# Optimization experiments

Hardware: AMD Instinct MI355X
Metric: run time of the kernel (lower is better)

The kernel has to match this reference:

```python
import jax, jax.numpy as jnp
import numpy as np

B, C, CO = 8, 32, 32            # batch, in_channels, out_channels
NIN, NOUT, D1, D2 = 16, 10, 512, 512  # MLP dims: 16 -> 512 -> 512 -> 10 (L=3)
NRC = (NIN + 2 * NOUT + 6) * C  # rc_inp feature dim = 42*C = 1344


def _conv1(x, W, b):
    # 1x1 Conv1d: x (b, Cin, N) -> (b, Cout, N)
    return jnp.einsum('oi,bin->bon', W, x) + b[None, :, None]


def _lin(x, W, b):
    return x @ W.T + b


def setup_inputs() -> dict:
    key = jax.random.key(0)
    ks = iter(jax.random.split(key, 64))
    def rn(shape, s=1.0):
        return jax.random.normal(next(ks), shape, dtype=jnp.float32) * s
    return {
        'w0': rn((B, C, D1, NIN)), 'w1': rn((B, C, D2, D1)), 'w2': rn((B, C, NOUT, D2)),
        'b0': rn((B, C, D1)), 'b1': rn((B, C, D2)), 'b2': rn((B, C, NOUT)),
        'W_w0_rpt': rn((NIN * CO, (NIN + 2) * C), 0.02), 'B_w0_rpt': rn((NIN * CO,), 0.02),
        'W_w0_rc': rn((NIN * CO, NRC), 0.02), 'B_w0_rc': rn((NIN * CO,), 0.02),
        'W_b0': rn((CO, (NIN + 2) * C), 0.02), 'B_b0': rn((CO,), 0.02),
        'W_b0_rc': rn((CO, NRC), 0.02), 'B_b0_rc': rn((CO,), 0.02),
        'W_l1': rn((CO, C), 0.02), 'B_l1': rn((CO,), 0.02),
        'W_l1_rc': rn((CO, NRC), 0.02), 'B_l1_rc': rn((CO,), 0.02),
        'W_l1_r': rn((CO, (3 + NIN) * C), 0.02), 'B_l1_r': rn((CO,), 0.02),
        'W_l1_c': rn((CO, (3 + NOUT) * C), 0.02), 'B_l1_c': rn((CO,), 0.02),
        'W_bias1': rn((CO, (3 + NOUT) * C), 0.02), 'B_bias1': rn((CO,), 0.02),
        'W_bias1_rc': rn((CO, NRC), 0.02), 'B_bias1_rc': rn((CO,), 0.02),
        'W_fin_cpt': rn((NOUT * CO, (NOUT + 1) * C), 0.02), 'B_fin_cpt': rn((NOUT * CO,), 0.02),
        'W_fin_rc': rn((NOUT * CO, NRC), 0.02), 'B_fin_rc': rn((NOUT * CO,), 0.02),
        'W_bfin_rc': rn((NOUT * CO, NRC), 0.02), 'B_bfin_rc': rn((NOUT * CO,), 0.02),
    }


def reference(w0, w1, w2, b0, b1, b2,
              W_w0_rpt, B_w0_rpt, W_w0_rc, B_w0_rc, W_b0, B_b0, W_b0_rc, B_b0_rc,
              W_l1, B_l1, W_l1_rc, B_l1_rc, W_l1_r, B_l1_r, W_l1_c, B_l1_c,
              W_bias1, B_bias1, W_bias1_rc, B_bias1_rc,
              W_fin_cpt, B_fin_cpt, W_fin_rc, B_fin_rc, W_bfin_rc, B_bfin_rc):
    b = w0.shape[0]
    cm0, cm1, cm2 = w0.mean(-1), w1.mean(-1), w2.mean(-1)  # col means (b,c,n_row)
    rm0, rm1, rm2 = w0.mean(-2), w1.mean(-2), w2.mean(-2)  # row means (b,c,n_col)
    rc = jnp.concatenate([
        w0.mean((-1, -2)), w1.mean((-1, -2)), w2.mean((-1, -2)),
        b0.mean(-1), b1.mean(-1), b2.mean(-1),
        rm0.reshape(b, -1), cm2.reshape(b, -1), b2.reshape(b, -1)], axis=-1)  # (b, NRC)
    # ---- layer 0 (row-pointwise + rc broadcast) ----
    rpt = jnp.concatenate([jnp.swapaxes(w0, -1, -2).reshape(b, C * NIN, D1), rm1, b0], axis=1)
    z0 = _conv1(rpt, W_w0_rpt, B_w0_rpt) + _lin(rc, W_w0_rc, B_w0_rc)[..., None]
    zw0 = jnp.swapaxes(z0.reshape(b, CO, NIN, D1), -1, -2)  # (b, co, D1, NIN)
    u0 = _conv1(rpt, W_b0, B_b0) + _lin(rc, W_b0_rc, B_b0_rc)[..., None]  # (b, co, D1)
    # ---- middle layer (pointwise + rc + row + col broadcasts) ----
    row_b = jnp.concatenate([rm1, cm0, b0, jnp.swapaxes(w0, -1, -2).reshape(b, C * NIN, D1)], axis=1)
    col_b = jnp.concatenate([cm1, b1, rm2, w2.reshape(b, C * NOUT, D2)], axis=1)
    zw1 = (jnp.einsum('oi,bihw->bohw', W_l1, w1) + B_l1[None, :, None, None]
           + _lin(rc, W_l1_rc, B_l1_rc)[..., None, None]
           + _conv1(row_b, W_l1_r, B_l1_r)[:, :, None, :]
           + _conv1(col_b, W_l1_c, B_l1_c)[:, :, :, None])  # (b, co, D2, D1)
    u1 = _conv1(col_b, W_bias1, B_bias1) + _lin(rc, W_bias1_rc, B_bias1_rc)[..., None]  # (b, co, D2)
    # ---- final layer (col-pointwise + rc broadcast) ----
    cpt = jnp.concatenate([w2.reshape(b, C * NOUT, D2), cm1], axis=1)
    zf = _conv1(cpt, W_fin_cpt, B_fin_cpt) + _lin(rc, W_fin_rc, B_fin_rc)[..., None]
    zw2 = zf.reshape(b, CO, NOUT, D2)
    u2 = _lin(rc, W_bfin_rc, B_bfin_rc).reshape(b, CO, NOUT)
    return (zw0, zw1, zw2, u0, u1, u2)
```

## Files before the change

kernel.cpp:

```cpp
#include <hip/hip_runtime.h>

#define OUT_ZW1 2097152u
#define OUT_ZW2 69206016u
#define OUT_U0  70516736u
#define OUT_U1  70647808u
#define OUT_U2  70778880u

#define WS_RM1P   0u
#define WS_CM1    524288u
#define WS_CM0    655360u
#define WS_RM2    786432u
#define WS_RCW1   917504u
#define WS_RC     918528u
#define WS_RTERM  929280u
#define WS_CTERM  1060352u
#define WS_W0T    1191424u
#define WS_TW0    3288576u
#define WS_TB0    3292672u
#define WS_TL1    3292928u
#define WS_TBIAS1 3293184u
#define WS_TFIN   3293440u

static __device__ __forceinline__ float wave_reduce(float v) {
#pragma unroll
  for (int off = 32; off > 0; off >>= 1) v += __shfl_down(v, off);
  return v;
}

__global__ __launch_bounds__(256) void ksetup(
    const float* __restrict__ w0, const float* __restrict__ w2,
    const float* __restrict__ b0, const float* __restrict__ b1,
    const float* __restrict__ b2, const float* __restrict__ w1,
    float* __restrict__ ws) {
  __shared__ float sred[16];
  __shared__ float stot;
  __shared__ float rpart[512];
  __shared__ float swsum[4];
  int tid = threadIdx.x, lane = tid & 63;
  int bx = blockIdx.x;

  if (bx < 256) {
    int bc = bx;
    int b = bc >> 5, c = bc & 31;
    float* rcb = ws + WS_RC + b * 1344;
    float* cm0 = ws + WS_CM0;
    float* rm2 = ws + WS_RM2;

    if (tid < 16) sred[tid] = 0.f;
    if (tid == 0) stot = 0.f;
    __syncthreads();
    {
      float rm0p[16];
#pragma unroll
      for (int k = 0; k < 16; ++k) rm0p[k] = 0.f;
      float tot = 0.f;
      for (int d = tid; d < 512; d += 256) {
        const float4* p = (const float4*)(w0 + ((size_t)bc * 512 + d) * 16);
        float s = 0.f;
#pragma unroll
        for (int q = 0; q < 4; ++q) {
          float4 v = p[q];
          s += v.x + v.y + v.z + v.w;
          rm0p[q * 4 + 0] += v.x; rm0p[q * 4 + 1] += v.y;
          rm0p[q * 4 + 2] += v.z; rm0p[q * 4 + 3] += v.w;
        }
        cm0[(size_t)bc * 512 + d] = s * (1.f / 16.f);
        tot += s;
      }
#pragma unroll
      for (int k = 0; k < 16; ++k) {
        float r = wave_reduce(rm0p[k]);
        if (lane == 0) atomicAdd(&sred[k], r);
      }
      float rt = wave_reduce(tot);
      if (lane == 0) atomicAdd(&stot, rt);
    }
    __syncthreads();
    if (tid < 16) rcb[192 + c * 16 + tid] = sred[tid] * (1.f / 512.f);
    if (tid == 0) rcb[c] = stot * (1.f / 8192.f);
    __syncthreads();

    if (tid < 10) sred[tid] = 0.f;
    if (tid == 0) stot = 0.f;
    __syncthreads();
    {
      float cm2p[10];
#pragma unroll
      for (int k = 0; k < 10; ++k) cm2p[k] = 0.f;
      float tot = 0.f;
      for (int d = tid; d < 512; d += 256) {
        float s = 0.f;
#pragma unroll
        for (int k = 0; k < 10; ++k) {
          float v = w2[((size_t)bc * 10 + k) * 512 + d];
          s += v; cm2p[k] += v;
        }
        rm2[(size_t)bc * 512 + d] = s * 0.1f;
        tot += s;
      }
#pragma unroll
      for (int k = 0; k < 10; ++k) {
        float r = wave_reduce(cm2p[k]);
        if (lane == 0) atomicAdd(&sred[k], r);
      }
      float rt = wave_reduce(tot);
      if (lane == 0) atomicAdd(&stot, rt);
    }
    __syncthreads();
    if (tid < 10) rcb[704 + c * 10 + tid] = sred[tid] * (1.f / 512.f);
    if (tid == 0) rcb[64 + c] = stot * (1.f / 5120.f);
    __syncthreads();

    if (tid < 2) sred[tid] = 0.f;
    __syncthreads();
    {
      float t0 = 0.f, t1 = 0.f;
      for (int d = tid; d < 512; d += 256) {
        t0 += b0[(size_t)bc * 512 + d];
        t1 += b1[(size_t)bc * 512 + d];
      }
      t0 = wave_reduce(t0); t1 = wave_reduce(t1);
      if (lane == 0) { atomicAdd(&sred[0], t0); atomicAdd(&sred[1], t1); }
    }
    __syncthreads();
    if (tid == 0) {
      rcb[96 + c] = sred[0] * (1.f / 512.f);
      rcb[128 + c] = sred[1] * (1.f / 512.f);
    }

    float vb2 = 0.f;
    if (tid < 10) {
      vb2 = b2[bc * 10 + tid];
      rcb[1024 + c * 10 + tid] = vb2;
    }
    if (tid < 64) {
      float s = wave_reduce(vb2);
      if (tid == 0) rcb[160 + c] = s * 0.1f;
    }
  } else if (bx < 1280) {
    int idx = bx - 256;
    int bc = idx >> 2, hc = idx & 3;
    int wid = tid >> 6;
    const float* base = w1 + (size_t)bc * 262144 + (size_t)hc * 65536;
    float col0 = 0.f, col1 = 0.f;
    for (int hl = 0; hl < 128; ++hl) {
      float2 x = *(const float2*)(base + hl * 512 + 2 * tid);
      col0 += x.x; col1 += x.y;
      float r = wave_reduce(x.x + x.y);
      if (lane == 0) rpart[hl * 4 + wid] = r;
    }
    __syncthreads();
    if (tid < 128) {
      float s = rpart[tid * 4] + rpart[tid * 4 + 1] + rpart[tid * 4 + 2] + rpart[tid * 4 + 3];
      ws[WS_CM1 + (size_t)bc * 512 + hc * 128 + tid] = s * (1.f / 512.f);
    }
    ws[WS_RM1P + (size_t)hc * 131072 + (size_t)bc * 512 + 2 * tid] = col0;
    ws[WS_RM1P + (size_t)hc * 131072 + (size_t)bc * 512 + 2 * tid + 1] = col1;
    float bt = wave_reduce(col0 + col1);
    if (lane == 0) swsum[wid] = bt;
    __syncthreads();
    if (tid == 0)
      ws[WS_RCW1 + hc * 256 + bc] = swsum[0] + swsum[1] + swsum[2] + swsum[3];
  } else {
    int bc = bx - 1280;
    int b = bc >> 5, c = bc & 31;
    for (int dd = 0; dd < 2; ++dd) {
      int d = tid + dd * 256;
      const float4* src = (const float4*)(w0 + ((size_t)bc * 512 + d) * 16);
      float4 v0 = src[0], v1 = src[1], v2 = src[2], v3 = src[3];
      float vals[16] = {v0.x, v0.y, v0.z, v0.w, v1.x, v1.y, v1.z, v1.w,
                        v2.x, v2.y, v2.z, v2.w, v3.x, v3.y, v3.z, v3.w};
#pragma unroll
      for (int k = 0; k < 16; ++k)
        ws[WS_W0T + ((size_t)(b * 512 + c * 16 + k)) * 512 + d] = vals[k];
    }
  }
}

__global__ __launch_bounds__(256) void krcgemm(
    float* __restrict__ ws,
    const float* __restrict__ W_w0_rc, const float* __restrict__ B_w0_rc,
    const float* __restrict__ W_b0_rc, const float* __restrict__ B_b0_rc,
    const float* __restrict__ W_l1_rc, const float* __restrict__ B_l1_rc,
    const float* __restrict__ W_bias1_rc, const float* __restrict__ B_bias1_rc,
    const float* __restrict__ W_fin_rc, const float* __restrict__ B_fin_rc,
    const float* __restrict__ W_bfin_rc, const float* __restrict__ B_bfin_rc,
    float* __restrict__ u2out) {
  int blk = blockIdx.x, tid = threadIdx.x;
  if (blk >= 2496) {
    int i = (blk - 2496) * 256 + tid;
    ws[WS_RM1P + i] = ws[WS_RM1P + i] + ws[WS_RM1P + 131072 + i] +
                      ws[WS_RM1P + 262144 + i] + ws[WS_RM1P + 393216 + i];
    return;
  }
  int b = blk / 312;
  int lane = tid & 63, wid = tid >> 6;
  int r = (blk % 312) * 4 + wid;
  __shared__ float rcs[1344];
  for (int j = tid; j < 1344; j += 256)
    if (j < 32 || j >= 64) rcs[j] = ws[WS_RC + b * 1344 + j];
  if (tid < 32)
    rcs[32 + tid] = (ws[WS_RCW1 + 0 * 256 + b * 32 + tid] +
                     ws[WS_RCW1 + 1 * 256 + b * 32 + tid] +
                     ws[WS_RCW1 + 2 * 256 + b * 32 + tid] +
                     ws[WS_RCW1 + 3 * 256 + b * 32 + tid]) * (1.f / 262144.f);
  __syncthreads();
  const float* W; const float* Bb; float* dst; int row;
  if (r < 512)      { W = W_w0_rc;    Bb = B_w0_rc;    row = r;       dst = ws + WS_TW0 + b * 512; }
  else if (r < 544) { W = W_b0_rc;    Bb = B_b0_rc;    row = r - 512; dst = ws + WS_TB0 + b * 32; }
  else if (r < 576) { W = W_l1_rc;    Bb = B_l1_rc;    row = r - 544; dst = ws + WS_TL1 + b * 32; }
  else if (r < 608) { W = W_bias1_rc; Bb = B_bias1_rc; row = r - 576; dst = ws + WS_TBIAS1 + b * 32; }
  else if (r < 928) { W = W_fin_rc;   Bb = B_fin_rc;   row = r - 608; dst = ws + WS_TFIN + b * 320; }
  else              { W = W_bfin_rc;  Bb = B_bfin_rc;  row = r - 928; dst = u2out + b * 320; }
  const float* wr = W + (size_t)row * 1344;
  float acc = 0.f;
  for (int j = lane; j < 1344; j += 64) acc += wr[j] * rcs[j];
  acc = wave_reduce(acc);
  if (lane == 0) dst[row] = acc + Bb[row];
}

#define FMA8x2(ACC_A, ACC_B, WA, WB, XA, XB)                                        \
  ACC_A[0] += WA.x * XA; ACC_A[1] += WA.y * XA; ACC_A[2] += WA.z * XA;              \
  ACC_A[3] += WA.w * XA; ACC_A[4] += WB.x * XA; ACC_A[5] += WB.y * XA;              \
  ACC_A[6] += WB.z * XA; ACC_A[7] += WB.w * XA;                                     \
  ACC_B[0] += WA.x * XB; ACC_B[1] += WA.y * XB; ACC_B[2] += WA.z * XB;              \
  ACC_B[3] += WA.w * XB; ACC_B[4] += WB.x * XB; ACC_B[5] += WB.y * XB;              \
  ACC_B[6] += WB.z * XB; ACC_B[7] += WB.w * XB;

__global__ __launch_bounds__(256) void kbig(
    const float* __restrict__ rm1, const float* __restrict__ cm0,
    const float* __restrict__ b0, const float* __restrict__ w0T,
    const float* __restrict__ W_l1_r, const float* __restrict__ B_l1_r,
    float* __restrict__ rterm,
    const float* __restrict__ cm1, const float* __restrict__ b1,
    const float* __restrict__ rm2, const float* __restrict__ w2,
    const float* __restrict__ W_l1_c, const float* __restrict__ B_l1_c,
    const float* __restrict__ B_l1, const float* __restrict__ t_l1,
    const float* __restrict__ W_bias1, const float* __restrict__ B_bias1,
    const float* __restrict__ t_bias1,
    float* __restrict__ cterm_full, float* __restrict__ u1out,
    const float* __restrict__ W_w0_rpt, const float* __restrict__ B_rpt,
    const float* __restrict__ W_b0, const float* __restrict__ B_b0w,
    const float* __restrict__ t_w0, const float* __restrict__ t_b0,
    const float* __restrict__ W_fin_cpt, const float* __restrict__ B_fin,
    const float* __restrict__ t_fin, float* __restrict__ out) {
  __shared__ float wlds[6656];
  int bid = blockIdx.x, tid = threadIdx.x;

  if (bid < 32) {
    int oy = bid & 3, b = bid >> 2;
    int p = 2 * tid;
    int o0 = oy * 8;
    for (int idx = tid; idx < 608 * 8; idx += 256) {
      int i = idx >> 3, oo = idx & 7;
      wlds[idx] = W_l1_r[(size_t)(o0 + oo) * 608 + i];
    }
    __syncthreads();
    float aA[8] = {0, 0, 0, 0, 0, 0, 0, 0};
    float aB[8] = {0, 0, 0, 0, 0, 0, 0, 0};
#pragma unroll 4
    for (int i = 0; i < 32; ++i) {
      float2 xv = *(const float2*)(rm1 + ((size_t)b * 32 + i) * 512 + p);
      float xa = xv.x * (1.f / 512.f), xb = xv.y * (1.f / 512.f);
      float4 wa = *(const float4*)&wlds[i * 8];
      float4 wb = *(const float4*)&wlds[i * 8 + 4];
      FMA8x2(aA, aB, wa, wb, xa, xb)
    }
#pragma unroll 4
    for (int i = 0; i < 32; ++i) {
      float2 xv = *(const float2*)(cm0 + ((size_t)b * 32 + i) * 512 + p);
      float4 wa = *(const float4*)&wlds[(32 + i) * 8];
      float4 wb = *(const float4*)&wlds[(32 + i) * 8 + 4];
      FMA8x2(aA, aB, wa, wb, xv.x, xv.y)
    }
#pragma unroll 4
    for (int i = 0; i < 32; ++i) {
      float2 xv = *(const float2*)(b0 + ((size_t)b * 32 + i) * 512 + p);
      float4 wa = *(const float4*)&wlds[(64 + i) * 8];
      float4 wb = *(const float4*)&wlds[(64 + i) * 8 + 4];
      FMA8x2(aA, aB, wa, wb, xv.x, xv.y)
    }
    const float* xp = w0T + (size_t)b * 512 * 512 + p;
#pragma unroll 4
    for (int i = 0; i < 512; ++i) {
      float2 xv = *(const float2*)(xp + (size_t)i * 512);
      float4 wa = *(const float4*)&wlds[(96 + i) * 8];
      float4 wb = *(const float4*)&wlds[(96 + i) * 8 + 4];
      FMA8x2(aA, aB, wa, wb, xv.x, xv.y)
    }
#pragma unroll
    for (int oo = 0; oo < 8; ++oo) {
      int o = o0 + oo;
      float bb = B_l1_r[o];
      *(float2*)(rterm + ((size_t)b * 32 + o) * 512 + p) = make_float2(aA[oo] + bb, aB[oo] + bb);
    }
  } else if (bid < 64) {
    int t = bid - 32;
    int oy = t & 3, b = t >> 2;
    int p = 2 * tid;
    int o0 = oy * 8;
    for (int idx = tid; idx < 416 * 8; idx += 256) {
      int i = idx >> 3, oo = idx & 7;
      wlds[idx] = W_l1_c[(size_t)(o0 + oo) * 416 + i];
      wlds[3328 + idx] = W_bias1[(size_t)(o0 + oo) * 416 + i];
    }
    __syncthreads();
    float cA[8] = {0, 0, 0, 0, 0, 0, 0, 0};
    float cB[8] = {0, 0, 0, 0, 0, 0, 0, 0};
    float uA[8] = {0, 0, 0, 0, 0, 0, 0, 0};
    float uB[8] = {0, 0, 0, 0, 0, 0, 0, 0};
#pragma unroll 2
    for (int i = 0; i < 32; ++i) {
      float2 xv = *(const float2*)(cm1 + ((size_t)b * 32 + i) * 512 + p);
      float4 wa = *(const float4*)&wlds[i * 8];
      float4 wb = *(const float4*)&wlds[i * 8 + 4];
      float4 va = *(const float4*)&wlds[3328 + i * 8];
      float4 vb = *(const float4*)&wlds[3328 + i * 8 + 4];
      FMA8x2(cA, cB, wa, wb, xv.x, xv.y)
      FMA8x2(uA, uB, va, vb, xv.x, xv.y)
    }
#pragma unroll 2
    for (int i = 0; i < 32; ++i) {
      float2 xv = *(const float2*)(b1 + ((size_t)b * 32 + i) * 512 + p);
      float4 wa = *(const float4*)&wlds[(32 + i) * 8];
      float4 wb = *(const float4*)&wlds[(32 + i) * 8 + 4];
      float4 va = *(const float4*)&wlds[3328 + (32 + i) * 8];
      float4 vb = *(const float4*)&wlds[3328 + (32 + i) * 8 + 4];
      FMA8x2(cA, cB, wa, wb, xv.x, xv.y)
      FMA8x2(uA, uB, va, vb, xv.x, xv.y)
    }
#pragma unroll 2
    for (int i = 0; i < 32; ++i) {
      float2 xv = *(const float2*)(rm2 + ((size_t)b * 32 + i) * 512 + p);
      float4 wa = *(const float4*)&wlds[(64 + i) * 8];
      float4 wb = *(const float4*)&wlds[(64 + i) * 8 + 4];
      float4 va = *(const float4*)&wlds[3328 + (64 + i) * 8];
      float4 vb = *(const float4*)&wlds[3328 + (64 + i) * 8 + 4];
      FMA8x2(cA, cB, wa, wb, xv.x, xv.y)
      FMA8x2(uA, uB, va, vb, xv.x, xv.y)
    }
    const float* xp = w2 + (size_t)b * 320 * 512 + p;
#pragma unroll 2
    for (int i = 0; i < 320; ++i) {
      float2 xv = *(const float2*)(xp + (size_t)i * 512);
      float4 wa = *(const float4*)&wlds[(96 + i) * 8];
      float4 wb = *(const float4*)&wlds[(96 + i) * 8 + 4];
      float4 va = *(const float4*)&wlds[3328 + (96 + i) * 8];
      float4 vb = *(const float4*)&wlds[3328 + (96 + i) * 8 + 4];
      FMA8x2(cA, cB, wa, wb, xv.x, xv.y)
      FMA8x2(uA, uB, va, vb, xv.x, xv.y)
    }
#pragma unroll
    for (int oo = 0; oo < 8; ++oo) {
      int o = o0 + oo;
      float cb = B_l1_c[o] + B_l1[o] + t_l1[b * 32 + o];
      float ub = B_bias1[o] + t_bias1[b * 32 + o];
      *(float2*)(cterm_full + ((size_t)b * 32 + o) * 512 + p) = make_float2(cA[oo] + cb, cB[oo] + cb);
      *(float2*)(u1out + ((size_t)b * 32 + o) * 512 + p) = make_float2(uA[oo] + ub, uB[oo] + ub);
    }
  } else if (bid < 608) {
    int t = bid - 64;
    int oc = t % 68, b = t / 68;
    bool isZ = oc < 64;
    int o0 = isZ ? oc * 8 : (oc - 64) * 8;
    const float* Wsrc = isZ ? W_w0_rpt : W_b0;
    for (int idx = tid; idx < 576 * 8; idx += 256) {
      int i = idx >> 3, oo = idx & 7;
      wlds[idx] = Wsrc[(size_t)(o0 + oo) * 576 + i];
    }
    __syncthreads();
    int d = 2 * tid;
    float aA[8] = {0, 0, 0, 0, 0, 0, 0, 0};
    float aB[8] = {0, 0, 0, 0, 0, 0, 0, 0};
    const float* xp = w0T + (size_t)b * 512 * 512 + d;
#pragma unroll 4
    for (int i = 0; i < 512; ++i) {
      float2 xv = *(const float2*)(xp + (size_t)i * 512);
      float4 wa = *(const float4*)&wlds[i * 8];
      float4 wb = *(const float4*)&wlds[i * 8 + 4];
      FMA8x2(aA, aB, wa, wb, xv.x, xv.y)
    }
#pragma unroll 4
    for (int i = 0; i < 32; ++i) {
      float2 xv = *(const float2*)(rm1 + ((size_t)b * 32 + i) * 512 + d);
      float xa = xv.x * (1.f / 512.f), xb = xv.y * (1.f / 512.f);
      float4 wa = *(const float4*)&wlds[(512 + i) * 8];
      float4 wb = *(const float4*)&wlds[(512 + i) * 8 + 4];
      FMA8x2(aA, aB, wa, wb, xa, xb)
    }
#pragma unroll 4
    for (int i = 0; i < 32; ++i) {
      float2 xv = *(const float2*)(b0 + ((size_t)b * 32 + i) * 512 + d);
      float4 wa = *(const float4*)&wlds[(544 + i) * 8];
      float4 wb = *(const float4*)&wlds[(544 + i) * 8 + 4];
      FMA8x2(aA, aB, wa, wb, xv.x, xv.y)
    }
    if (isZ) {
#pragma unroll
      for (int oo = 0; oo < 8; ++oo) {
        int o = o0 + oo, co = o >> 4, k = o & 15;
        float bb = B_rpt[o] + t_w0[b * 512 + o];
        size_t base = (((size_t)b * 32 + co) * 512 + d) * 16 + k;
        out[base] = aA[oo] + bb;
        out[base + 16] = aB[oo] + bb;
      }
    } else {
#pragma unroll
      for (int oo = 0; oo < 8; ++oo) {
        int o = o0 + oo;
        float bb = B_b0w[o] + t_b0[b * 32 + o];
        *(float2*)(out + OUT_U0 + ((size_t)b * 32 + o) * 512 + d) =
            make_float2(aA[oo] + bb, aB[oo] + bb);
      }
    }
  } else {
    int t = bid - 608;
    int oc = t % 40, b = t / 40;
    int o0 = oc * 8;
    for (int idx = tid; idx < 352 * 8; idx += 256) {
      int i = idx >> 3, oo = idx & 7;
      wlds[idx] = W_fin_cpt[(size_t)(o0 + oo) * 352 + i];
    }
    __syncthreads();
    int d = 2 * tid;
    float aA[8] = {0, 0, 0, 0, 0, 0, 0, 0};
    float aB[8] = {0, 0, 0, 0, 0, 0, 0, 0};
    const float* xp = w2 + (size_t)b * 320 * 512 + d;
#pragma unroll 4
    for (int i = 0; i < 320; ++i) {
      float2 xv = *(const float2*)(xp + (size_t)i * 512);
      float4 wa = *(const float4*)&wlds[i * 8];
      float4 wb = *(const float4*)&wlds[i * 8 + 4];
      FMA8x2(aA, aB, wa, wb, xv.x, xv.y)
    }
#pragma unroll 4
    for (int i = 0; i < 32; ++i) {
      float2 xv = *(const float2*)(cm1 + ((size_t)b * 32 + i) * 512 + d);
      float4 wa = *(const float4*)&wlds[(320 + i) * 8];
      float4 wb = *(const float4*)&wlds[(320 + i) * 8 + 4];
      FMA8x2(aA, aB, wa, wb, xv.x, xv.y)
    }
#pragma unroll
    for (int oo = 0; oo < 8; ++oo) {
      int o = o0 + oo;
      float bb = B_fin[o] + t_fin[b * 320 + o];
      *(float2*)(out + OUT_ZW2 + ((size_t)b * 320 + o) * 512 + d) =
          make_float2(aA[oo] + bb, aB[oo] + bb);
    }
  }
}

__global__ __launch_bounds__(256) void kzw1(
    const float* __restrict__ w1, const float* __restrict__ W_l1,
    const float* __restrict__ rterm, const float* __restrict__ cterm,
    float* __restrict__ out) {
  __shared__ float wl[1024];
  int hp = blockIdx.x, b = blockIdx.y;
  int t = threadIdx.x;
  for (int i = t; i < 1024; i += 256) wl[(i & 31) * 32 + (i >> 5)] = W_l1[i];
  __syncthreads();
  int h0 = hp * 2;
  int hoff = t >> 7;
  int w = (t & 127) * 4;
  float4 acc[32];
#pragma unroll
  for (int o = 0; o < 32; ++o) acc[o] = make_float4(0.f, 0.f, 0.f, 0.f);
  const float* src = w1 + ((size_t)b * 32 * 512 + h0) * 512 + 4 * t;
#pragma unroll 4
  for (int i = 0; i < 32; ++i) {
    float4 x = *(const float4*)(src + (size_t)i * 262144);
    const float* wp = wl + i * 32;
#pragma unroll
    for (int o = 0; o < 32; ++o) {
      acc[o].x += wp[o] * x.x;
      acc[o].y += wp[o] * x.y;
      acc[o].z += wp[o] * x.z;
      acc[o].w += wp[o] * x.w;
    }
  }
  int h = h0 + hoff;
#pragma unroll
  for (int o = 0; o < 32; ++o) {
    float cf = cterm[((size_t)b * 32 + o) * 512 + h];
    float4 rt = *(const float4*)(rterm + ((size_t)b * 32 + o) * 512 + w);
    float4 res = make_float4(acc[o].x + rt.x + cf, acc[o].y + rt.y + cf,
                             acc[o].z + rt.z + cf, acc[o].w + rt.w + cf);
    *(float4*)(out + (size_t)OUT_ZW1 + (((size_t)b * 32 + o) * 512 + h) * 512 + w) = res;
  }
}

extern "C" void kernel_launch(void* const* d_in, const int* in_sizes, int n_in,
                              void* d_out, int out_size, void* d_ws, size_t ws_size,
                              hipStream_t stream) {
  const float* w0 = (const float*)d_in[0];
  const float* w1 = (const float*)d_in[1];
  const float* w2 = (const float*)d_in[2];
  const float* b0 = (const float*)d_in[3];
  const float* b1 = (const float*)d_in[4];
  const float* b2 = (const float*)d_in[5];
  const float* W_w0_rpt = (const float*)d_in[6];
  const float* B_w0_rpt = (const float*)d_in[7];
  const float* W_w0_rc = (const float*)d_in[8];
  const float* B_w0_rc = (const float*)d_in[9];
  const float* W_b0 = (const float*)d_in[10];
  const float* B_b0 = (const float*)d_in[11];
  const float* W_b0_rc = (const float*)d_in[12];
  const float* B_b0_rc = (const float*)d_in[13];
  const float* W_l1 = (const float*)d_in[14];
  const float* B_l1 = (const float*)d_in[15];
  const float* W_l1_rc = (const float*)d_in[16];
  const float* B_l1_rc = (const float*)d_in[17];
  const float* W_l1_r = (const float*)d_in[18];
  const float* B_l1_r = (const float*)d_in[19];
  const float* W_l1_c = (const float*)d_in[20];
  const float* B_l1_c = (const float*)d_in[21];
  const float* W_bias1 = (const float*)d_in[22];
  const float* B_bias1 = (const float*)d_in[23];
  const float* W_bias1_rc = (const float*)d_in[24];
  const float* B_bias1_rc = (const float*)d_in[25];
  const float* W_fin_cpt = (const float*)d_in[26];
  const float* B_fin_cpt = (const float*)d_in[27];
  const float* W_fin_rc = (const float*)d_in[28];
  const float* B_fin_rc = (const float*)d_in[29];
  const float* W_bfin_rc = (const float*)d_in[30];
  const float* B_bfin_rc = (const float*)d_in[31];
  float* ws = (float*)d_ws;
  float* out = (float*)d_out;

  ksetup<<<dim3(1536), 256, 0, stream>>>(w0, w2, b0, b1, b2, w1, ws);

  krcgemm<<<dim3(3008), 256, 0, stream>>>(
      ws, W_w0_rc, B_w0_rc, W_b0_rc, B_b0_rc, W_l1_rc, B_l1_rc, W_bias1_rc,
      B_bias1_rc, W_fin_rc, B_fin_rc, W_bfin_rc, B_bfin_rc, out + OUT_U2);

  kbig<<<dim3(928), 256, 0, stream>>>(
      ws + WS_RM1P, ws + WS_CM0, b0, ws + WS_W0T, W_l1_r, B_l1_r, ws + WS_RTERM,
      ws + WS_CM1, b1, ws + WS_RM2, w2, W_l1_c, B_l1_c, B_l1, ws + WS_TL1, W_bias1,
      B_bias1, ws + WS_TBIAS1, ws + WS_CTERM, out + OUT_U1,
      W_w0_rpt, B_w0_rpt, W_b0, B_b0, ws + WS_TW0, ws + WS_TB0,
      W_fin_cpt, B_fin_cpt, ws + WS_TFIN, out);

  kzw1<<<dim3(256, 8), 256, 0, stream>>>(w1, W_l1, ws + WS_RTERM, ws + WS_CTERM, out);
  (void)in_sizes; (void)n_in; (void)out_size; (void)ws_size;
}
```

Before: 365.0 us.

## Stage big-input chunks in LDS with coalesced float4 loads in kbig

Replaces the per-thread strided float2 global reads of w0T and w2 in kbig with a chunked loop that cooperatively loads 16-row tiles into shared memory as float4, along with the matching 16x8 weight slice, before running the FMAs. The small side inputs keep a reduced preloaded weight table. The rm1 partial reduction now writes to a separate workspace region instead of in place, so the pointer passed to kbig changes. This adds two barriers per chunk and raises LDS use per block in exchange for wider, more coalesced loads and less LDS weight preloading.

```diff
diff --git a/kernel.cpp b/kernel.cpp
--- a/kernel.cpp
+++ b/kernel.cpp
@@ -20,12 +20,21 @@
 #define WS_TL1    3292928u
 #define WS_TBIAS1 3293184u
 #define WS_TFIN   3293440u
+#define WS_RM1F   3296000u
 
 static __device__ __forceinline__ float wave_reduce(float v) {
 #pragma unroll
   for (int off = 32; off > 0; off >>= 1) v += __shfl_down(v, off);
   return v;
 }
+
+#define FMA8x2(ACC_A, ACC_B, WA, WB, XA, XB)                                        \
+  ACC_A[0] += WA.x * XA; ACC_A[1] += WA.y * XA; ACC_A[2] += WA.z * XA;              \
+  ACC_A[3] += WA.w * XA; ACC_A[4] += WB.x * XA; ACC_A[5] += WB.y * XA;              \
+  ACC_A[6] += WB.z * XA; ACC_A[7] += WB.w * XA;                                     \
+  ACC_B[0] += WA.x * XB; ACC_B[1] += WA.y * XB; ACC_B[2] += WA.z * XB;              \
+  ACC_B[3] += WA.w * XB; ACC_B[4] += WB.x * XB; ACC_B[5] += WB.y * XB;              \
+  ACC_B[6] += WB.z * XB; ACC_B[7] += WB.w * XB;
 
 __global__ __launch_bounds__(256) void ksetup(
     const float* __restrict__ w0, const float* __restrict__ w2,
@@ -189,7 +198,7 @@
   int blk = blockIdx.x, tid = threadIdx.x;
   if (blk >= 2496) {
     int i = (blk - 2496) * 256 + tid;
-    ws[WS_RM1P + i] = ws[WS_RM1P + i] + ws[WS_RM1P + 131072 + i] +
+    ws[WS_RM1F + i] = ws[WS_RM1P + i] + ws[WS_RM1P + 131072 + i] +
                       ws[WS_RM1P + 262144 + i] + ws[WS_RM1P + 393216 + i];
     return;
   }
@@ -219,14 +228,6 @@
   if (lane == 0) dst[row] = acc + Bb[row];
 }
 
-#define FMA8x2(ACC_A, ACC_B, WA, WB, XA, XB)                                        \
-  ACC_A[0] += WA.x * XA; ACC_A[1] += WA.y * XA; ACC_A[2] += WA.z * XA;              \
-  ACC_A[3] += WA.w * XA; ACC_A[4] += WB.x * XA; ACC_A[5] += WB.y * XA;              \
-  ACC_A[6] += WB.z * XA; ACC_A[7] += WB.w * XA;                                     \
-  ACC_B[0] += WA.x * XB; ACC_B[1] += WA.y * XB; ACC_B[2] += WA.z * XB;              \
-  ACC_B[3] += WA.w * XB; ACC_B[4] += WB.x * XB; ACC_B[5] += WB.y * XB;              \
-  ACC_B[6] += WB.z * XB; ACC_B[7] += WB.w * XB;
-
 __global__ __launch_bounds__(256) void kbig(
     const float* __restrict__ rm1, const float* __restrict__ cm0,
     const float* __restrict__ b0, const float* __restrict__ w0T,
@@ -244,110 +245,137 @@
     const float* __restrict__ t_w0, const float* __restrict__ t_b0,
     const float* __restrict__ W_fin_cpt, const float* __restrict__ B_fin,
     const float* __restrict__ t_fin, float* __restrict__ out) {
-  __shared__ float wlds[6656];
+  __shared__ float xt[8192];
+  __shared__ float wch[256];
+  __shared__ float wext[1536];
   int bid = blockIdx.x, tid = threadIdx.x;
+  int d = 2 * tid;
+
+#define CHUNK_LOOP(NCH, XP, WSRC, WLEN, WOFF)                                       \
+  for (int ch = 0; ch < (NCH); ++ch) {                                              \
+    const float4* g4 = (const float4*)((XP) + (size_t)ch * 16 * 512);               \
+    float4* x4 = (float4*)xt;                                                       \
+    _Pragma("unroll")                                                               \
+    for (int k = 0; k < 8; ++k) x4[tid + k * 256] = g4[tid + k * 256];              \
+    if (tid < 128) {                                                                \
+      int i = tid >> 3, oo = tid & 7;                                               \
+      wch[tid] = (WSRC)[(size_t)(o0 + oo) * (WLEN) + (WOFF) + ch * 16 + i];         \
+    }                                                                               \
+    __syncthreads();                                                                \
+    _Pragma("unroll")                                                               \
+    for (int i = 0; i < 16; ++i) {                                                  \
+      float2 xv = *(const float2*)&xt[i * 512 + d];                                 \
+      float4 wa = *(const float4*)&wch[i * 8];                                      \
+      float4 wb = *(const float4*)&wch[i * 8 + 4];                                  \
+      FMA8x2(aA, aB, wa, wb, xv.x, xv.y)                                            \
+    }                                                                               \
+    __syncthreads();                                                                \
+  }
 
   if (bid < 32) {
     int oy = bid & 3, b = bid >> 2;
-    int p = 2 * tid;
     int o0 = oy * 8;
-    for (int idx = tid; idx < 608 * 8; idx += 256) {
+    for (int idx = tid; idx < 768; idx += 256) {
       int i = idx >> 3, oo = idx & 7;
-      wlds[idx] = W_l1_r[(size_t)(o0 + oo) * 608 + i];
-    }
-    __syncthreads();
+      wext[idx] = W_l1_r[(size_t)(o0 + oo) * 608 + i];
+    }
     float aA[8] = {0, 0, 0, 0, 0, 0, 0, 0};
     float aB[8] = {0, 0, 0, 0, 0, 0, 0, 0};
-#pragma unroll 4
-    for (int i = 0; i < 32; ++i) {
-      float2 xv = *(const float2*)(rm1 + ((size_t)b * 32 + i) * 512 + p);
+    const float* xp = w0T + (size_t)b * 512 * 512;
+    CHUNK_LOOP(32, xp, W_l1_r, 608, 96)
+#pragma unroll 4
+    for (int i = 0; i < 32; ++i) {
+      float2 xv = *(const float2*)(rm1 + ((size_t)b * 32 + i) * 512 + d);
       float xa = xv.x * (1.f / 512.f), xb = xv.y * (1.f / 512.f);
-      float4 wa = *(const float4*)&wlds[i * 8];
-      float4 wb = *(const float4*)&wlds[i * 8 + 4];
+      float4 wa = *(const float4*)&wext[i * 8];
+      float4 wb = *(const float4*)&wext[i * 8 + 4];
       FMA8x2(aA, aB, wa, wb, xa, xb)
     }
 #pragma unroll 4
     for (int i = 0; i < 32; ++i) {
-      float2 xv = *(const float2*)(cm0 + ((size_t)b * 32 + i) * 512 + p);
-      float4 wa = *(const float4*)&wlds[(32 + i) * 8];
-      float4 wb = *(const float4*)&wlds[(32 + i) * 8 + 4];
-      FMA8x2(aA, aB, wa, wb, xv.x, xv.y)
-    }
-#pragma unroll 4
-    for (int i = 0; i < 32; ++i) {
-      float2 xv = *(const float2*)(b0 + ((size_t)b * 32 + i) * 512 + p);
-      float4 wa = *(const float4*)&wlds[(64 + i) * 8];
-      float4 wb = *(const float4*)&wlds[(64 + i) * 8 + 4];
-      FMA8x2(aA, aB, wa, wb, xv.x, xv.y)
-    }
-    const float* xp = w0T + (size_t)b * 512 * 512 + p;
-#pragma unroll 4
-    for (int i = 0; i < 512; ++i) {
-      float2 xv = *(const float2*)(xp + (size_t)i * 512);
-      float4 wa = *(const float4*)&wlds[(96 + i) * 8];
-      float4 wb = *(const float4*)&wlds[(96 + i) * 8 + 4];
+      float2 xv = *(const float2*)(cm0 + ((size_t)b * 32 + i) * 512 + d);
+      float4 wa = *(const float4*)&wext[(32 + i) * 8];
+      float4 wb = *(const float4*)&wext[(32 + i) * 8 + 4];
+      FMA8x2(aA, aB, wa, wb, xv.x, xv.y)
+    }
+#pragma unroll 4
+    for (int i = 0; i < 32; ++i) {
+      float2 xv = *(const float2*)(b0 + ((size_t)b * 32 + i) * 512 + d);
+      float4 wa = *(const float4*)&wext[(64 + i) * 8];
+      float4 wb = *(const float4*)&wext[(64 + i) * 8 + 4];
       FMA8x2(aA, aB, wa, wb, xv.x, xv.y)
     }
 #pragma unroll
     for (int oo = 0; oo < 8; ++oo) {
       int o = o0 + oo;
       float bb = B_l1_r[o];
-      *(float2*)(rterm + ((size_t)b * 32 + o) * 512 + p) = make_float2(aA[oo] + bb, aB[oo] + bb);
+      *(float2*)(rterm + ((size_t)b * 32 + o) * 512 + d) = make_float2(aA[oo] + bb, aB[oo] + bb);
     }
   } else if (bid < 64) {
     int t = bid - 32;
     int oy = t & 3, b = t >> 2;
-    int p = 2 * tid;
     int o0 = oy * 8;
-    for (int idx = tid; idx < 416 * 8; idx += 256) {
+    for (int idx = tid; idx < 768; idx += 256) {
       int i = idx >> 3, oo = idx & 7;
-      wlds[idx] = W_l1_c[(size_t)(o0 + oo) * 416 + i];
-      wlds[3328 + idx] = W_bias1[(size_t)(o0 + oo) * 416 + i];
-    }
-    __syncthreads();
-    float cA[8] = {0, 0, 0, 0, 0, 0, 0, 0};
-    float cB[8] = {0, 0, 0, 0, 0, 0, 0, 0};
+      wext[idx] = W_l1_c[(size_t)(o0 + oo) * 416 + i];
+      wext[768 + idx] = W_bias1[(size_t)(o0 + oo) * 416 + i];
+    }
+    float aA[8] = {0, 0, 0, 0, 0, 0, 0, 0};
+    float aB[8] = {0, 0, 0, 0, 0, 0, 0, 0};
     float uA[8] = {0, 0, 0, 0, 0, 0, 0, 0};
     float uB[8] = {0, 0, 0, 0, 0, 0, 0, 0};
+    const float* xp = w2 + (size_t)b * 320 * 512;
+    for (int ch = 0; ch < 20; ++ch) {
+      const float4* g4 = (const float4*)(xp + (size_t)ch * 16 * 512);
+      float4* x4 = (float4*)xt;
+#pragma unroll
+      for (int k = 0; k < 8; ++k) x4[tid + k * 256] = g4[tid + k * 256];
+      if (tid < 128) {
+        int i = tid >> 3, oo = tid & 7;
+        wch[tid] = W_l1_c[(size_t)(o0 + oo) * 416 + 96 + ch * 16 + i];
+        wch[128 + tid] = W_bias1[(size_t)(o0 + oo) * 416 + 96 + ch * 16 + i];
+      }
+      __syncthreads();
+#pragma unroll
+      for (int i = 0; i < 16; ++i) {
+        float2 xv = *(const float2*)&xt[i * 512 + d];
+        float4 wa = *(const float4*)&wch[i * 8];
+        float4 wb = *(const float4*)&wch[i * 8 + 4];
+        float4 va = *(const float4*)&wch[128 + i * 8];
+        float4 vb = *(const float4*)&wch[128 + i * 8 + 4];
+        FMA8x2(aA, aB, wa, wb, xv.x, xv.y)
+        FMA8x2(uA, uB, va, vb, xv.x, xv.y)
+      }
+      __syncthreads();
+    }
 #pragma unroll 2
     for (int i = 0; i < 32; ++i) {
-      float2 xv = *(const float2*)(cm1 + ((size_t)b * 32 + i) * 512 + p);
-      float4 wa = *(const float4*)&wlds[i * 8];
-      float4 wb = *(const float4*)&wlds[i * 8 + 4];
-      float4 va = *(const float4*)&wlds[3328 + i * 8];
-      float4 vb = *(const float4*)&wlds[3328 + i * 8 + 4];
-      FMA8x2(cA, cB, wa, wb, xv.x, xv.y)
+      float2 xv = *(const float2*)(cm1 + ((size_t)b * 32 + i) * 512 + d);
+      float4 wa = *(const float4*)&wext[i * 8];
+      float4 wb = *(const float4*)&wext[i * 8 + 4];
+      float4 va = *(const float4*)&wext[768 + i * 8];
+      float4 vb = *(const float4*)&wext[768 + i * 8 + 4];
+      FMA8x2(aA, aB, wa, wb, xv.x, xv.y)
       FMA8x2(uA, uB, va, vb, xv.x, xv.y)
     }
 #pragma unroll 2
     for (int i = 0; i < 32; ++i) {
-      float2 xv = *(const float2*)(b1 + ((size_t)b * 32 + i) * 512 + p);
-      float4 wa = *(const float4*)&wlds[(32 + i) * 8];
-      float4 wb = *(const float4*)&wlds[(32 + i) * 8 + 4];
-      float4 va = *(const float4*)&wlds[3328 + (32 + i) * 8];
-      float4 vb = *(const float4*)&wlds[3328 + (32 + i) * 8 + 4];
-      FMA8x2(cA, cB, wa, wb, xv.x, xv.y)
+      float2 xv = *(const float2*)(b1 + ((size_t)b * 32 + i) * 512 + d);
+      float4 wa = *(const float4*)&wext[(32 + i) * 8];
+      float4 wb = *(const float4*)&wext[(32 + i) * 8 + 4];
+      float4 va = *(const float4*)&wext[768 + (32 + i) * 8];
+      float4 vb = *(const float4*)&wext[768 + (32 + i) * 8 + 4];
+      FMA8x2(aA, aB, wa, wb, xv.x, xv.y)
       FMA8x2(uA, uB, va, vb, xv.x, xv.y)
     }
 #pragma unroll 2
     for (int i = 0; i < 32; ++i) {
-      float2 xv = *(const float2*)(rm2 + ((size_t)b * 32 + i) * 512 + p);
-      float4 wa = *(const float4*)&wlds[(64 + i) * 8];
-      float4 wb = *(const float4*)&wlds[(64 + i) * 8 + 4];
-      float4 va = *(const float4*)&wlds[3328 + (64 + i) * 8];
-      float4 vb = *(const float4*)&wlds[3328 + (64 + i) * 8 + 4];
-      FMA8x2(cA, cB, wa, wb, xv.x, xv.y)
-      FMA8x2(uA, uB, va, vb, xv.x, xv.y)
-    }
-    const float* xp = w2 + (size_t)b * 320 * 512 + p;
-#pragma unroll 2
-    for (int i = 0; i < 320; ++i) {
-      float2 xv = *(const float2*)(xp + (size_t)i * 512);
-      float4 wa = *(const float4*)&wlds[(96 + i) * 8];
-      float4 wb = *(const float4*)&wlds[(96 + i) * 8 + 4];
-      float4 va = *(const float4*)&wlds[3328 + (96 + i) * 8];
-      float4 vb = *(const float4*)&wlds[3328 + (96 + i) * 8 + 4];
-      FMA8x2(cA, cB, wa, wb, xv.x, xv.y)
+      float2 xv = *(const float2*)(rm2 + ((size_t)b * 32 + i) * 512 + d);
+      float4 wa = *(const float4*)&wext[(64 + i) * 8];
+      float4 wb = *(const float4*)&wext[(64 + i) * 8 + 4];
+      float4 va = *(const float4*)&wext[768 + (64 + i) * 8];
+      float4 vb = *(const float4*)&wext[768 + (64 + i) * 8 + 4];
+      FMA8x2(aA, aB, wa, wb, xv.x, xv.y)
       FMA8x2(uA, uB, va, vb, xv.x, xv.y)
     }
 #pragma unroll
@@ -355,8 +383,8 @@
       int o = o0 + oo;
       float cb = B_l1_c[o] + B_l1[o] + t_l1[b * 32 + o];
       float ub = B_bias1[o] + t_bias1[b * 32 + o];
-      *(float2*)(cterm_full + ((size_t)b * 32 + o) * 512 + p) = make_float2(cA[oo] + cb, cB[oo] + cb);
-      *(float2*)(u1out + ((size_t)b * 32 + o) * 512 + p) = make_float2(uA[oo] + ub, uB[oo] + ub);
+      *(float2*)(cterm_full + ((size_t)b * 32 + o) * 512 + d) = make_float2(aA[oo] + cb, aB[oo] + cb);
+      *(float2*)(u1out + ((size_t)b * 32 + o) * 512 + d) = make_float2(uA[oo] + ub, uB[oo] + ub);
     }
   } else if (bid < 608) {
     int t = bid - 64;
@@ -364,35 +392,27 @@
     bool isZ = oc < 64;
     int o0 = isZ ? oc * 8 : (oc - 64) * 8;
     const float* Wsrc = isZ ? W_w0_rpt : W_b0;
-    for (int idx = tid; idx < 576 * 8; idx += 256) {
+    for (int idx = tid; idx < 512; idx += 256) {
       int i = idx >> 3, oo = idx & 7;
-      wlds[idx] = Wsrc[(size_t)(o0 + oo) * 576 + i];
-    }
-    __syncthreads();
-    int d = 2 * tid;
+      wext[idx] = Wsrc[(size_t)(o0 + oo) * 576 + 512 + i];
+    }
     float aA[8] = {0, 0, 0, 0, 0, 0, 0, 0};
     float aB[8] = {0, 0, 0, 0, 0, 0, 0, 0};
-    const float* xp = w0T + (size_t)b * 512 * 512 + d;
-#pragma unroll 4
-    for (int i = 0; i < 512; ++i) {
-      float2 xv = *(const float2*)(xp + (size_t)i * 512);
-      float4 wa = *(const float4*)&wlds[i * 8];
-      float4 wb = *(const float4*)&wlds[i * 8 + 4];
-      FMA8x2(aA, aB, wa, wb, xv.x, xv.y)
-    }
+    const float* xp = w0T + (size_t)b * 512 * 512;
+    CHUNK_LOOP(32, xp, Wsrc, 576, 0)
 #pragma unroll 4
     for (int i = 0; i < 32; ++i) {
       float2 xv = *(const float2*)(rm1 + ((size_t)b * 32 + i) * 512 + d);
       float xa = xv.x * (1.f / 512.f), xb = xv.y * (1.f / 512.f);
-      float4 wa = *(const float4*)&wlds[(512 + i) * 8];
-      float4 wb = *(const float4*)&wlds[(512 + i) * 8 + 4];
+      float4 wa = *(const float4*)&wext[i * 8];
+      float4 wb = *(const float4*)&wext[i * 8 + 4];
       FMA8x2(aA, aB, wa, wb, xa, xb)
     }
 #pragma unroll 4
     for (int i = 0; i < 32; ++i) {
       float2 xv = *(const float2*)(b0 + ((size_t)b * 32 + i) * 512 + d);
-      float4 wa = *(const float4*)&wlds[(544 + i) * 8];
-      float4 wb = *(const float4*)&wlds[(544 + i) * 8 + 4];
+      float4 wa = *(const float4*)&wext[(32 + i) * 8];
+      float4 wb = *(const float4*)&wext[(32 + i) * 8 + 4];
       FMA8x2(aA, aB, wa, wb, xv.x, xv.y)
     }
     if (isZ) {
@@ -417,27 +437,19 @@
     int t = bid - 608;
     int oc = t % 40, b = t / 40;
     int o0 = oc * 8;
-    for (int idx = tid; idx < 352 * 8; idx += 256) {
+    for (int idx = tid; idx < 256; idx += 256) {
       int i = idx >> 3, oo = idx & 7;
-      wlds[idx] = W_fin_cpt[(size_t)(o0 + oo) * 352 + i];
-    }
-    __syncthreads();
-    int d = 2 * tid;
+      wext[idx] = W_fin_cpt[(size_t)(o0 + oo) * 352 + 320 + i];
+    }
     float aA[8] = {0, 0, 0, 0, 0, 0, 0, 0};
     float aB[8] = {0, 0, 0, 0, 0, 0, 0, 0};
-    const float* xp = w2 + (size_t)b * 320 * 512 + d;
-#pragma unroll 4
-    for (int i = 0; i < 320; ++i) {
-      float2 xv = *(const float2*)(xp + (size_t)i * 512);
-      float4 wa = *(const float4*)&wlds[i * 8];
-      float4 wb = *(const float4*)&wlds[i * 8 + 4];
-      FMA8x2(aA, aB, wa, wb, xv.x, xv.y)
-    }
+    const float* xp = w2 + (size_t)b * 320 * 512;
+    CHUNK_LOOP(20, xp, W_fin_cpt, 352, 0)
 #pragma unroll 4
     for (int i = 0; i < 32; ++i) {
       float2 xv = *(const float2*)(cm1 + ((size_t)b * 32 + i) * 512 + d);
-      float4 wa = *(const float4*)&wlds[(320 + i) * 8];
-      float4 wb = *(const float4*)&wlds[(320 + i) * 8 + 4];
+      float4 wa = *(const float4*)&wext[i * 8];
+      float4 wb = *(const float4*)&wext[i * 8 + 4];
       FMA8x2(aA, aB, wa, wb, xv.x, xv.y)
     }
 #pragma unroll
@@ -448,6 +460,7 @@
           make_float2(aA[oo] + bb, aB[oo] + bb);
     }
   }
+#undef CHUNK_LOOP
 }
 
 __global__ __launch_bounds__(256) void kzw1(
@@ -534,7 +547,7 @@
       B_bias1_rc, W_fin_rc, B_fin_rc, W_bfin_rc, B_bfin_rc, out + OUT_U2);
 
   kbig<<<dim3(928), 256, 0, stream>>>(
-      ws + WS_RM1P, ws + WS_CM0, b0, ws + WS_W0T, W_l1_r, B_l1_r, ws + WS_RTERM,
+      ws + WS_RM1F, ws + WS_CM0, b0, ws + WS_W0T, W_l1_r, B_l1_r, ws + WS_RTERM,
       ws + WS_CM1, b1, ws + WS_RM2, w2, W_l1_c, B_l1_c, B_l1, ws + WS_TL1, W_bias1,
       B_bias1, ws + WS_TBIAS1, ws + WS_CTERM, out + OUT_U1,
       W_w0_rpt, B_w0_rpt, W_b0, B_b0, ws + WS_TW0, ws + WS_TB0,
```

New measurement: 359.5 us. Within noise of the previous version (-1.5%).
